# Performance work log

Measured on AMD Instinct MI355X. Metric: run time of the kernel, lower is better.

Reference implementation:

```python
import jax, jax.numpy as jnp
import numpy as np

EMBED_DIM = 1024
NUM_HEADS = 16
D_K = EMBED_DIM // NUM_HEADS
BATCH, SEQ = 4, 2048


def setup_inputs() -> dict:
    key = jax.random.key(0)
    ks = jax.random.split(key, 6)
    s = 1.0 / np.sqrt(EMBED_DIM)
    return {
        "x": jax.random.normal(ks[0], (BATCH, SEQ, EMBED_DIM), dtype=jnp.float32),
        "mask": jnp.ones((BATCH, SEQ), dtype=jnp.int32),
        "Wq": jax.random.uniform(ks[1], (EMBED_DIM, EMBED_DIM), jnp.float32, -s, s),
        "Wk": jax.random.uniform(ks[2], (EMBED_DIM, EMBED_DIM), jnp.float32, -s, s),
        "Wv": jax.random.uniform(ks[3], (EMBED_DIM, EMBED_DIM), jnp.float32, -s, s),
        "Wo": jax.random.uniform(ks[4], (EMBED_DIM, EMBED_DIM), jnp.float32, -s, s),
    }


def reference(x, mask, Wq, Wk, Wv, Wo):
    B, S, E = x.shape
    H, Dk = NUM_HEADS, D_K
    # nn.Linear: y = x @ W.T ; reshape to [B, H, S, Dk]
    def proj(W):
        return jnp.einsum('bse,fe->bsf', x, W).reshape(B, S, H, Dk).transpose(0, 2, 1, 3)
    q, k, v = proj(Wq), proj(Wk), proj(Wv)
    scores = jnp.einsum('bhqd,bhkd->bhqk', q, k) / jnp.sqrt(jnp.float32(Dk))
    # key-padding mask: [B, S] -> [B, 1, 1, S]; 0 means masked with -inf
    scores = jnp.where(mask[:, None, None, :] == 0, -jnp.inf, scores)
    attn = jax.nn.softmax(scores, axis=-1)  # dropout is identity (p=0 / eval)
    out = jnp.einsum('bhqk,bhkd->bhqd', attn, v)
    out = out.transpose(0, 2, 1, 3).reshape(B, S, E)
    return jnp.einsum('bse,fe->bsf', out, Wo)
```

## Files before the change

kernel.cpp:

```cpp
#include <hip/hip_runtime.h>

typedef __attribute__((ext_vector_type(8))) __bf16   bf16x8;
typedef __attribute__((ext_vector_type(8))) _Float16 f16x8;
typedef __attribute__((ext_vector_type(4))) _Float16 f16x4;
typedef __attribute__((ext_vector_type(2))) __fp16   h16x2;
typedef __attribute__((ext_vector_type(4))) __fp16   h16x4;
typedef __attribute__((ext_vector_type(4))) float    f32x4;

#define MFMA_BF16 __builtin_amdgcn_mfma_f32_16x16x32_bf16
#define MFMA_F16  __builtin_amdgcn_mfma_f32_16x16x32_f16

__global__ __launch_bounds__(256)
void cast_bf16(const float* __restrict__ src, __bf16* __restrict__ dst, int n8)
{
    int i = blockIdx.x * 256 + threadIdx.x;
    if (i >= n8) return;
    float4 v0 = *(const float4*)(src + (size_t)i * 8);
    float4 v1 = *(const float4*)(src + (size_t)i * 8 + 4);
    float xs[8] = {v0.x, v0.y, v0.z, v0.w, v1.x, v1.y, v1.z, v1.w};
    bf16x8 h8;
    #pragma unroll
    for (int j = 0; j < 8; j++) h8[j] = (__bf16)xs[j];
    *(bf16x8*)(dst + (size_t)i * 8) = h8;
}

__global__ __launch_bounds__(256)
void mask_bias(const int* __restrict__ mask, float* __restrict__ bias, int n)
{
    int i = blockIdx.x * 256 + threadIdx.x;
    if (i < n) bias[i] = mask[i] ? 0.f : -30000.f;
}

#define GEMM_DECLS                                                          \
    __shared__ __bf16 Ah[128][40], Bh[128][40];                             \
    const int t    = threadIdx.x;                                           \
    const int lane = t & 63;                                                \
    const int wid  = t >> 6;                                                \
    const int l15  = lane & 15;                                             \
    const int lg   = lane >> 4;                                             \
    const int wr   = wid >> 1, wc = wid & 1;

#define GEMM_LOOP(Ag, Bg, m0, brow0, K)                                     \
    f32x4 acc[4][4];                                                        \
    _Pragma("unroll")                                                       \
    for (int i = 0; i < 4; i++)                                             \
        _Pragma("unroll")                                                   \
        for (int jj = 0; jj < 4; jj++)                                      \
            _Pragma("unroll")                                               \
            for (int r = 0; r < 4; r++) acc[i][jj][r] = 0.f;                \
    for (int k0 = 0; k0 < K; k0 += 32) {                                    \
        __syncthreads();                                                    \
        _Pragma("unroll")                                                   \
        for (int i = 0; i < 2; i++) {                                       \
            int id = t + 256 * i;                                           \
            int row = id >> 2, cc = id & 3;                                 \
            *(bf16x8*)&Ah[row][cc*8] =                                      \
                *(const bf16x8*)(Ag + (size_t)(m0 + row) * K + k0 + cc*8);  \
            *(bf16x8*)&Bh[row][cc*8] =                                      \
                *(const bf16x8*)(Bg + (size_t)(brow0 + row) * K + k0 + cc*8);\
        }                                                                   \
        __syncthreads();                                                    \
        bf16x8 ah[4];                                                       \
        _Pragma("unroll")                                                   \
        for (int mr = 0; mr < 4; mr++)                                      \
            ah[mr] = *(const bf16x8*)&Ah[wr*64 + mr*16 + l15][lg*8];        \
        _Pragma("unroll")                                                   \
        for (int nr = 0; nr < 4; nr++) {                                    \
            bf16x8 bh = *(const bf16x8*)&Bh[wc*64 + nr*16 + l15][lg*8];     \
            _Pragma("unroll")                                               \
            for (int mr = 0; mr < 4; mr++)                                  \
                acc[mr][nr] = MFMA_BF16(ah[mr], bh, acc[mr][nr], 0, 0, 0);  \
        }                                                                   \
    }

__global__ __launch_bounds__(256, 4)
void gemm_qkv(const __bf16* __restrict__ xh, const __bf16* __restrict__ w3,
              __bf16* __restrict__ qh, __bf16* __restrict__ kh,
              _Float16* __restrict__ vh)
{
    GEMM_DECLS
    const int K = 1024, N = 1024;
    const int m0     = blockIdx.x * 128;
    const int by     = blockIdx.y;
    const int region = by >> 3;
    const int n0     = (by & 7) * 128;
    const int brow0  = region * 1024 + n0;
    GEMM_LOOP(xh, w3, m0, brow0, K)

    constexpr float QSCALE = 0.18033688011112f;
    #pragma unroll
    for (int mr = 0; mr < 4; mr++)
    #pragma unroll
    for (int r = 0; r < 4; r++) {
        int row = m0 + wr*64 + mr*16 + lg*4 + r;
        #pragma unroll
        for (int nr = 0; nr < 4; nr++) {
            int col = n0 + wc*64 + nr*16 + l15;
            size_t off = (size_t)row * N + col;
            float v = acc[mr][nr][r];
            if (region == 0)      qh[off] = (__bf16)(v * QSCALE);
            else if (region == 1) kh[off] = (__bf16)v;
            else                  vh[off] = (_Float16)v;
        }
    }
}

__global__ __launch_bounds__(256, 4)
void gemm_out(const __bf16* __restrict__ aoh, const __bf16* __restrict__ woh,
              float* __restrict__ out, int M, int N, int K)
{
    GEMM_DECLS
    const int m0 = blockIdx.x * 128, n0 = blockIdx.y * 128;
    GEMM_LOOP(aoh, woh, m0, n0, K)

    #pragma unroll
    for (int mr = 0; mr < 4; mr++)
    #pragma unroll
    for (int r = 0; r < 4; r++) {
        int row = m0 + wr*64 + mr*16 + lg*4 + r;
        #pragma unroll
        for (int nr = 0; nr < 4; nr++) {
            int col = n0 + wc*64 + nr*16 + l15;
            out[(size_t)row * N + col] = acc[mr][nr][r];
        }
    }
}

__global__ __launch_bounds__(256, 2)
void attn_bf16(const __bf16* __restrict__ Qg, const __bf16* __restrict__ Kg,
               const _Float16* __restrict__ Vg, const float* __restrict__ biasg,
               __bf16* AO)
{
    const int S = 2048, E = 1024;
    __shared__ __bf16   Kh[64][72];
    __shared__ _Float16 Vt[80][72];
    __shared__ _Float16 Ps[128][72];

    const int tid  = threadIdx.x;
    const int lane = tid & 63;
    const int wid  = tid >> 6;
    const int l15  = lane & 15;
    const int lg   = lane >> 4;

    const int fid = blockIdx.x;
    const int xcd = fid & 7;
    const int j   = fid >> 3;
    const int bh  = xcd * 8 + (j >> 4);
    const int qb  = j & 15;
    const int h   = bh & 15;
    const int b   = bh >> 4;
    const int q0  = qb * 128;
    const size_t base = (size_t)b * S * E + (size_t)h * 64;

    {
        _Float16* vones = &Vt[64][0];
        for (int i = tid; i < 16 * 72; i += 256) vones[i] = (_Float16)1.0f;
    }

    bf16x8 qf[2][2];
    #pragma unroll
    for (int mg = 0; mg < 2; mg++) {
        size_t qoff = base + (size_t)(q0 + wid*32 + mg*16 + l15) * E;
        #pragma unroll
        for (int kc = 0; kc < 2; kc++)
            qf[mg][kc] = *(const bf16x8*)(Qg + qoff + kc*32 + lg*8);
    }

    f32x4 o[2][4], osum[2];
    #pragma unroll
    for (int mg = 0; mg < 2; mg++) {
        #pragma unroll
        for (int nt = 0; nt < 4; nt++)
            #pragma unroll
            for (int r = 0; r < 4; r++) o[mg][nt][r] = 0.f;
        #pragma unroll
        for (int r = 0; r < 4; r++) osum[mg][r] = 0.f;
    }

    bf16x8 kpre[2]; f16x8 vpre[2];
    #pragma unroll
    for (int i = 0; i < 2; i++) {
        int id = tid + 256 * i, row = id >> 3, scc = id & 7;
        size_t g0 = base + (size_t)(row) * E + scc * 8;
        kpre[i] = *(const bf16x8*)(Kg + g0);
        vpre[i] = *(const f16x8*)(Vg + g0);
    }

    const int NT = S / 64;
    for (int t = 0; t < NT; t++) {
        const int k0 = t * 64;
        __syncthreads();

        #pragma unroll
        for (int i = 0; i < 2; i++) {
            int id = tid + 256 * i, row = id >> 3, scc = id & 7;
            *(bf16x8*)&Kh[(row & 3) * 16 + (row >> 2)][scc*8] = kpre[i];
            int cbase = ((row >> 3) ^ scc) * 8 + (row & 7);
            #pragma unroll
            for (int jj = 0; jj < 8; jj++)
                Vt[scc*8 + jj][cbase] = vpre[i][jj];
        }

        if (t + 1 < NT) {
            #pragma unroll
            for (int i = 0; i < 2; i++) {
                int id = tid + 256 * i, row = id >> 3, scc = id & 7;
                size_t gn = base + (size_t)(k0 + 64 + row) * E + scc * 8;
                kpre[i] = *(const bf16x8*)(Kg + gn);
                vpre[i] = *(const f16x8*)(Vg + gn);
            }
        }
        __syncthreads();

        f32x4 bias4 = *(const f32x4*)(biasg + b * S + k0 + l15 * 4);
        f32x4 sf[2][4];
        #pragma unroll
        for (int mg = 0; mg < 2; mg++)
            #pragma unroll
            for (int nt = 0; nt < 4; nt++)
                #pragma unroll
                for (int r = 0; r < 4; r++) sf[mg][nt][r] = bias4[nt];

        #pragma unroll
        for (int kc = 0; kc < 2; kc++)
            #pragma unroll
            for (int nt = 0; nt < 4; nt++) {
                bf16x8 kb = *(const bf16x8*)&Kh[nt*16 + l15][kc*32 + lg*8];
                #pragma unroll
                for (int mg = 0; mg < 2; mg++)
                    sf[mg][nt] = MFMA_BF16(qf[mg][kc], kb, sf[mg][nt], 0, 0, 0);
            }

        #pragma unroll
        for (int mg = 0; mg < 2; mg++)
            #pragma unroll
            for (int r = 0; r < 4; r++) {
                int rowp = wid*32 + mg*16 + lg*4 + r;
                float p0 = __builtin_amdgcn_exp2f(sf[mg][0][r]);
                float p1 = __builtin_amdgcn_exp2f(sf[mg][1][r]);
                float p2 = __builtin_amdgcn_exp2f(sf[mg][2][r]);
                float p3 = __builtin_amdgcn_exp2f(sf[mg][3][r]);
                h16x2 a = __builtin_amdgcn_cvt_pkrtz(p0, p1);
                h16x2 c = __builtin_amdgcn_cvt_pkrtz(p2, p3);
                h16x4 pv4 = __builtin_shufflevector(a, c, 0, 1, 2, 3);
                *(h16x4*)&Ps[rowp][l15 * 4] = pv4;
            }

        asm volatile("s_waitcnt lgkmcnt(0)" ::: "memory");
        __builtin_amdgcn_sched_barrier(0);

        #pragma unroll
        for (int kc = 0; kc < 2; kc++) {
            f16x8 pa0 = *(const f16x8*)&Ps[wid*32 +      l15][kc*32 + lg*8];
            f16x8 pa1 = *(const f16x8*)&Ps[wid*32 + 16 + l15][kc*32 + lg*8];
            #pragma unroll
            for (int nt = 0; nt < 4; nt++) {
                int c8p = (kc*4 + lg) ^ (nt*2 + (l15 >> 3));
                f16x8 vb = *(const f16x8*)&Vt[nt*16 + l15][c8p*8];
                o[0][nt] = MFMA_F16(pa0, vb, o[0][nt], 0, 0, 0);
                o[1][nt] = MFMA_F16(pa1, vb, o[1][nt], 0, 0, 0);
            }
            f16x8 vb1 = *(const f16x8*)&Vt[64 + l15][(kc*4 + lg)*8];
            osum[0] = MFMA_F16(pa0, vb1, osum[0], 0, 0, 0);
            osum[1] = MFMA_F16(pa1, vb1, osum[1], 0, 0, 0);
        }
    }

    float inv[2][4];
    #pragma unroll
    for (int mg = 0; mg < 2; mg++)
        #pragma unroll
        for (int r = 0; r < 4; r++) inv[mg][r] = 1.0f / osum[mg][r];

    unsigned short* Pu = (unsigned short*)&Ps[0][0];
    __syncthreads();
    #pragma unroll
    for (int mg = 0; mg < 2; mg++)
        #pragma unroll
        for (int r = 0; r < 4; r++)
            #pragma unroll
            for (int nt = 0; nt < 4; nt++) {
                __bf16 v = (__bf16)(o[mg][nt][r] * inv[mg][r]);
                Pu[(wid*32 + mg*16 + lg*4 + r) * 72 + nt*16 + l15] =
                    *(unsigned short*)&v;
            }
    __syncthreads();
    #pragma unroll
    for (int i = 0; i < 4; i++) {
        int u   = tid + 256 * i;
        int row = u >> 3, c8 = u & 7;
        bf16x8 v8;
        #pragma unroll
        for (int jj = 0; jj < 8; jj++) {
            unsigned short us = Pu[row * 72 + c8*8 + jj];
            v8[jj] = *(__bf16*)&us;
        }
        *(bf16x8*)(AO + base + (size_t)(q0 + row) * E + c8 * 8) = v8;
    }
}

extern "C" void kernel_launch(void* const* d_in, const int* in_sizes, int n_in,
                              void* d_out, int out_size, void* d_ws, size_t ws_size,
                              hipStream_t stream)
{
    const float* x    = (const float*)d_in[0];
    const int*   mask = (const int*)  d_in[1];
    const float* Wq   = (const float*)d_in[2];
    const float* Wk   = (const float*)d_in[3];
    const float* Wv   = (const float*)d_in[4];
    const float* Wo   = (const float*)d_in[5];
    float* out = (float*)d_out;

    const int B = 4, S = 2048, E = 1024;
    const int M = B * S;
    const size_t SZ  = (size_t)M * E;
    const size_t WSZ = (size_t)E * E;
    const size_t PB  = SZ * sizeof(__bf16);

    char* ws = (char*)d_ws;
    __bf16*   qh = (__bf16*)(ws);
    __bf16*   kh = (__bf16*)(ws + PB);
    _Float16* vh = (_Float16*)(ws + 2*PB);
    __bf16*   xh = (__bf16*)(ws + 3*PB);
    __bf16*   w3 = (__bf16*)(ws + 4*PB);
    __bf16*   wo = (__bf16*)(ws + 4*PB + 3*WSZ*sizeof(__bf16));
    float*    bs = (float*)(ws + 4*PB + 4*WSZ*sizeof(__bf16));

    const int n8x = (int)(SZ / 8);
    const int n8w = (int)(WSZ / 8);

    cast_bf16<<<n8x/256, 256, 0, stream>>>(x,  xh, n8x);
    cast_bf16<<<n8w/256, 256, 0, stream>>>(Wq, w3,           n8w);
    cast_bf16<<<n8w/256, 256, 0, stream>>>(Wk, w3 + WSZ,     n8w);
    cast_bf16<<<n8w/256, 256, 0, stream>>>(Wv, w3 + 2*WSZ,   n8w);
    cast_bf16<<<n8w/256, 256, 0, stream>>>(Wo, wo, n8w);
    mask_bias<<<(B*S)/256, 256, 0, stream>>>(mask, bs, B*S);

    gemm_qkv<<<dim3(M/128, 24), dim3(256), 0, stream>>>(xh, w3, qh, kh, vh);

    attn_bf16<<<dim3(1024), dim3(256), 0, stream>>>(qh, kh, vh, bs, qh);

    gemm_out<<<dim3(M/128, E/128), dim3(256), 0, stream>>>(qh, wo, out, M, E, E);
}
```

Before: 223.7 us.

## Keep softmax probabilities in registers by transposing QK^T MFMA operands

Swaps the operands of the QK^T MFMA so each lane's score accumulator lands directly in the layout the PV MFMA needs as its A operand. The P tile then goes straight from registers into the f16 MFMA, and the Ps shared-memory staging, its LDS wait and its reads are removed. The V transpose swizzle and the bias load pattern are changed to match the new key ordering. Shared memory is merged into one aliased buffer, which cuts LDS use and may allow higher occupancy, at the cost of more intricate index math that must stay consistent.

```diff
diff --git a/kernel.cpp b/kernel.cpp
--- a/kernel.cpp
+++ b/kernel.cpp
@@ -2,9 +2,8 @@
 
 typedef __attribute__((ext_vector_type(8))) __bf16   bf16x8;
 typedef __attribute__((ext_vector_type(8))) _Float16 f16x8;
-typedef __attribute__((ext_vector_type(4))) _Float16 f16x4;
 typedef __attribute__((ext_vector_type(2))) __fp16   h16x2;
-typedef __attribute__((ext_vector_type(4))) __fp16   h16x4;
+typedef __attribute__((ext_vector_type(8))) __fp16   h16x8;
 typedef __attribute__((ext_vector_type(4))) float    f32x4;
 
 #define MFMA_BF16 __builtin_amdgcn_mfma_f32_16x16x32_bf16
@@ -132,9 +131,9 @@
                __bf16* AO)
 {
     const int S = 2048, E = 1024;
-    __shared__ __bf16   Kh[64][72];
-    __shared__ _Float16 Vt[80][72];
-    __shared__ _Float16 Ps[128][72];
+    __shared__ __align__(16) char smem[20736];
+    __bf16   (*Kh)[72] = (__bf16 (*)[72])smem;
+    _Float16 (*Vt)[72] = (_Float16 (*)[72])(smem + 9216);
 
     const int tid  = threadIdx.x;
     const int lane = tid & 63;
@@ -194,11 +193,13 @@
         #pragma unroll
         for (int i = 0; i < 2; i++) {
             int id = tid + 256 * i, row = id >> 3, scc = id & 7;
-            *(bf16x8*)&Kh[(row & 3) * 16 + (row >> 2)][scc*8] = kpre[i];
-            int cbase = ((row >> 3) ^ scc) * 8 + (row & 7);
+            *(bf16x8*)&Kh[row][scc*8] = kpre[i];
+            int sg   = ((row & 12) >> 2) * 8 + ((row >> 4) & 1) * 4
+                     + (row & 3) + (row & 32);
+            int colw = (((sg >> 3) ^ scc) << 3) + (sg & 7);
             #pragma unroll
             for (int jj = 0; jj < 8; jj++)
-                Vt[scc*8 + jj][cbase] = vpre[i][jj];
+                Vt[scc*8 + jj][colw] = vpre[i][jj];
         }
 
         if (t + 1 < NT) {
@@ -212,57 +213,58 @@
         }
         __syncthreads();
 
-        f32x4 bias4 = *(const f32x4*)(biasg + b * S + k0 + l15 * 4);
         f32x4 sf[2][4];
         #pragma unroll
-        for (int mg = 0; mg < 2; mg++)
-            #pragma unroll
-            for (int nt = 0; nt < 4; nt++)
-                #pragma unroll
-                for (int r = 0; r < 4; r++) sf[mg][nt][r] = bias4[nt];
-
+        for (int kvb = 0; kvb < 4; kvb++) {
+            f32x4 bias4 = *(const f32x4*)(biasg + b * S + k0 + kvb*16 + lg*4);
+            sf[0][kvb] = bias4;
+            sf[1][kvb] = bias4;
+        }
         #pragma unroll
         for (int kc = 0; kc < 2; kc++)
             #pragma unroll
-            for (int nt = 0; nt < 4; nt++) {
-                bf16x8 kb = *(const bf16x8*)&Kh[nt*16 + l15][kc*32 + lg*8];
+            for (int kvb = 0; kvb < 4; kvb++) {
+                bf16x8 kb = *(const bf16x8*)&Kh[kvb*16 + l15][kc*32 + lg*8];
                 #pragma unroll
                 for (int mg = 0; mg < 2; mg++)
-                    sf[mg][nt] = MFMA_BF16(qf[mg][kc], kb, sf[mg][nt], 0, 0, 0);
-            }
-
-        #pragma unroll
-        for (int mg = 0; mg < 2; mg++)
-            #pragma unroll
-            for (int r = 0; r < 4; r++) {
-                int rowp = wid*32 + mg*16 + lg*4 + r;
-                float p0 = __builtin_amdgcn_exp2f(sf[mg][0][r]);
-                float p1 = __builtin_amdgcn_exp2f(sf[mg][1][r]);
-                float p2 = __builtin_amdgcn_exp2f(sf[mg][2][r]);
-                float p3 = __builtin_amdgcn_exp2f(sf[mg][3][r]);
-                h16x2 a = __builtin_amdgcn_cvt_pkrtz(p0, p1);
-                h16x2 c = __builtin_amdgcn_cvt_pkrtz(p2, p3);
-                h16x4 pv4 = __builtin_shufflevector(a, c, 0, 1, 2, 3);
-                *(h16x4*)&Ps[rowp][l15 * 4] = pv4;
-            }
-
-        asm volatile("s_waitcnt lgkmcnt(0)" ::: "memory");
-        __builtin_amdgcn_sched_barrier(0);
-
-        #pragma unroll
-        for (int kc = 0; kc < 2; kc++) {
-            f16x8 pa0 = *(const f16x8*)&Ps[wid*32 +      l15][kc*32 + lg*8];
-            f16x8 pa1 = *(const f16x8*)&Ps[wid*32 + 16 + l15][kc*32 + lg*8];
+                    sf[mg][kvb] = MFMA_BF16(kb, qf[mg][kc], sf[mg][kvb], 0, 0, 0);
+            }
+
+        f16x8 pa[2][2];
+        #pragma unroll
+        for (int mg = 0; mg < 2; mg++) {
+            float p[4][4];
+            #pragma unroll
+            for (int kvb = 0; kvb < 4; kvb++)
+                #pragma unroll
+                for (int r = 0; r < 4; r++)
+                    p[kvb][r] = __builtin_amdgcn_exp2f(sf[mg][kvb][r]);
+            #pragma unroll
+            for (int hh = 0; hh < 2; hh++) {
+                h16x2 c0 = __builtin_amdgcn_cvt_pkrtz(p[2*hh][0],   p[2*hh][1]);
+                h16x2 c1 = __builtin_amdgcn_cvt_pkrtz(p[2*hh][2],   p[2*hh][3]);
+                h16x2 c2 = __builtin_amdgcn_cvt_pkrtz(p[2*hh+1][0], p[2*hh+1][1]);
+                h16x2 c3 = __builtin_amdgcn_cvt_pkrtz(p[2*hh+1][2], p[2*hh+1][3]);
+                h16x8 t8 = __builtin_shufflevector(
+                    __builtin_shufflevector(c0, c1, 0, 1, 2, 3),
+                    __builtin_shufflevector(c2, c3, 0, 1, 2, 3),
+                    0, 1, 2, 3, 4, 5, 6, 7);
+                pa[mg][hh] = __builtin_bit_cast(f16x8, t8);
+            }
+        }
+
+        #pragma unroll
+        for (int hh = 0; hh < 2; hh++) {
             #pragma unroll
             for (int nt = 0; nt < 4; nt++) {
-                int c8p = (kc*4 + lg) ^ (nt*2 + (l15 >> 3));
+                int c8p = (hh*4 + lg) ^ (nt*2 + (l15 >> 3));
                 f16x8 vb = *(const f16x8*)&Vt[nt*16 + l15][c8p*8];
-                o[0][nt] = MFMA_F16(pa0, vb, o[0][nt], 0, 0, 0);
-                o[1][nt] = MFMA_F16(pa1, vb, o[1][nt], 0, 0, 0);
-            }
-            f16x8 vb1 = *(const f16x8*)&Vt[64 + l15][(kc*4 + lg)*8];
-            osum[0] = MFMA_F16(pa0, vb1, osum[0], 0, 0, 0);
-            osum[1] = MFMA_F16(pa1, vb1, osum[1], 0, 0, 0);
+                o[0][nt] = MFMA_F16(pa[0][hh], vb, o[0][nt], 0, 0, 0);
+                o[1][nt] = MFMA_F16(pa[1][hh], vb, o[1][nt], 0, 0, 0);
+            }
+            f16x8 vb1 = *(const f16x8*)&Vt[64 + l15][(hh*4 + lg)*8];
+            osum[0] = MFMA_F16(pa[0][hh], vb1, osum[0], 0, 0, 0);
+            osum[1] = MFMA_F16(pa[1][hh], vb1, osum[1], 0, 0, 0);
         }
     }
 
@@ -272,7 +274,7 @@
         #pragma unroll
         for (int r = 0; r < 4; r++) inv[mg][r] = 1.0f / osum[mg][r];
 
-    unsigned short* Pu = (unsigned short*)&Ps[0][0];
+    unsigned short* Pu = (unsigned short*)smem;
     __syncthreads();
     #pragma unroll
     for (int mg = 0; mg < 2; mg++)
```

Measured after the change: 206.8 us. 1.08x faster.
